# Optimization experiments

Hardware: AMD Instinct MI355X
Metric: run time of the kernel (lower is better)

## Reference

```python
import jax, jax.numpy as jnp
import numpy as np

B, M, N, F, H = 4, 512, 1024, 256, 256
K, K2, KC, RADIUS = 8, 4, 16, 0.5
EPS = 1e-5


def _cdist(a, b):
    d2 = (jnp.sum(a * a, -1)[..., :, None] + jnp.sum(b * b, -1)[..., None, :]
          - 2.0 * jnp.einsum('bnd,bmd->bnm', a, b))
    return jnp.sqrt(jnp.maximum(d2, 0.0))


def _scf_oe(xyz):
    # spherical coords (r, theta, phi) relative to cloud centroid -> (B,3,Npts)
    rel = xyz - jnp.mean(xyz, axis=1, keepdims=True)
    r = jnp.sqrt(jnp.sum(rel * rel, -1) + 1e-8)
    theta = jnp.arccos(jnp.clip(rel[..., 2] / r, -1.0, 1.0))
    phi = jnp.arctan2(rel[..., 1], rel[..., 0])
    return jnp.stack([r, theta, phi], axis=1)


def _knn_desc(xyz):
    # per-point SCF descriptor: sorted distances to KC nearest neighbors
    d = _cdist(xyz, xyz)
    return jnp.sort(d, axis=-1)[..., 1:KC + 1]


def _inorm(x):
    # InstanceNorm1d, affine=False: normalize over last dim per (b, row)
    mu = jnp.mean(x, -1, keepdims=True)
    var = jnp.var(x, -1, keepdims=True)
    return (x - mu) / jnp.sqrt(var + EPS)


def _conv1x1(x, W, g, b):
    # Conv2d 1x1 + BN(affine) + ReLU on (B,C,N,K)
    y = jnp.einsum('bcnk,oc->bonk', x, W)
    return jax.nn.relu(g[:, None, None] * y + b[:, None, None])


def _conv12(x, W, g, b):
    # Conv2d kernel (1,2) stride (1,2) + BN(affine) + ReLU on (B,C,N,P)
    Bb, C, Nn, P = x.shape
    xr = x.reshape(Bb, C, Nn, P // 2, 2)
    y = jnp.einsum('bcnpt,oct->bonp', xr, W)
    return jax.nn.relu(g[:, None, None] * y + b[:, None, None])


def _pointsift(xyz, feat, params):
    # PointSIFT OE: nearest neighbor in each of 8 octants within radius
    w1, g1, b1, w2, g2, b2, w3, g3, b3 = params
    Bb, Nn, _ = xyz.shape
    diff = xyz[:, None, :, :] - xyz[:, :, None, :]  # diff[b,i,j] = xyz[j]-xyz[i]
    d2 = jnp.sum(diff * diff, -1)
    octant = ((diff[..., 0] > 0).astype(jnp.int32) * 4
              + (diff[..., 1] > 0).astype(jnp.int32) * 2
              + (diff[..., 2] > 0).astype(jnp.int32))
    base = jnp.broadcast_to(jnp.arange(Nn)[None, :], (Bb, Nn))
    idxs = []
    for c in range(8):  # fixed small structural loop
        m = (octant == c) & (d2 <= RADIUS * RADIUS) & (d2 > 0)
        dm = jnp.where(m, d2, jnp.inf)
        j = jnp.argmin(dm, -1)
        valid = jnp.isfinite(jnp.min(dm, -1))
        idxs.append(jnp.where(valid, j, base))
    idx = jnp.stack(idxs, -1)  # (B,N,8)
    gxyz = jax.vmap(lambda p, i: p[i])(xyz, idx) - xyz[:, :, None, :]
    gfeat = jax.vmap(lambda f, i: f[i])(feat, idx)
    g = jnp.concatenate([gxyz, gfeat], -1).transpose(0, 3, 1, 2)  # (B,3+C,N,8)
    g = _conv12(g, w1, g1, b1)
    g = _conv12(g, w2, g2, b2)
    g = _conv12(g, w3, g3, b3)
    return g[..., 0]  # (B,C,N)


def setup_inputs():
    key = jax.random.key(0)
    ks = iter(jax.random.split(key, 64))
    rn = lambda shape, s=0.05: jax.random.normal(next(ks), shape, dtype=jnp.float32) * s
    ones = lambda shape: jnp.ones(shape, jnp.float32)
    zeros = lambda shape: jnp.zeros(shape, jnp.float32)
    inp = {
        'template_feature': rn((B, F, M), 1.0),
        'search_feature': rn((B, F, N), 1.0),
        'template_xyz': rn((B, M, 3), 1.0),
        'search_xyz': rn((B, N, 3), 1.0),
        'template_bc': rn((B, M, 9), 1.0),
        'search_bc': rn((B, N, 9), 1.0),
        'mlp_w1': rn((H, F + 3)), 'mlp_g1': ones(H), 'mlp_b1': zeros(H),
        'mlp_w2': rn((H, H)), 'mlp_g2': ones(H), 'mlp_b2': zeros(H),
        'mlp_w3': rn((H, H)), 'mlp_g3': ones(H), 'mlp_b3': zeros(H),
        'fea_w1': rn((F, H)), 'fea_g1': ones(F), 'fea_b1': zeros(F),
        'fea_w2': rn((F, F)), 'fea_bias2': zeros(F),
        'attn_wqkv': rn((3 * F, F)),
        'pos_w1': rn((64, 12)), 'pos_b1': zeros(64),
        'pos_w2': rn((F, 64)), 'pos_b2': zeros(F),
        'amlp_w1': rn((4 * F, F)), 'amlp_b1': zeros(4 * F),
        'amlp_w2': rn((F, 4 * F)), 'amlp_b2': zeros(F),
        'oe1_w1': rn((F, F + 3, 2)), 'oe1_g1': ones(F), 'oe1_b1': zeros(F),
        'oe1_w2': rn((F, F, 2)), 'oe1_g2': ones(F), 'oe1_b2': zeros(F),
        'oe1_w3': rn((F, F, 2)), 'oe1_g3': ones(F), 'oe1_b3': zeros(F),
        'oe2_w1': rn((F, F + 3, 2)), 'oe2_g1': ones(F), 'oe2_b1': zeros(F),
        'oe2_w2': rn((F, F, 2)), 'oe2_g2': ones(F), 'oe2_b2': zeros(F),
        'oe2_w3': rn((F, F, 2)), 'oe2_g3': ones(F), 'oe2_b3': zeros(F),
    }
    return inp


def reference(template_feature, search_feature, template_xyz, search_xyz, template_bc, search_bc,
              mlp_w1, mlp_g1, mlp_b1, mlp_w2, mlp_g2, mlp_b2, mlp_w3, mlp_g3, mlp_b3,
              fea_w1, fea_g1, fea_b1, fea_w2, fea_bias2,
              attn_wqkv, pos_w1, pos_b1, pos_w2, pos_b2, amlp_w1, amlp_b1, amlp_w2, amlp_b2,
              oe1_w1, oe1_g1, oe1_b1, oe1_w2, oe1_g2, oe1_b2, oe1_w3, oe1_g3, oe1_b3,
              oe2_w1, oe2_g1, oe2_b1, oe2_w2, oe2_g2, oe2_b2, oe2_w3, oe2_g3, oe2_b3):
    # ---- box-cloud distance + candidate pruning ----
    dist_bc = _cdist(template_bc, search_bc)  # (B,M,N)
    t_box = jnp.concatenate([template_xyz.transpose(0, 2, 1), template_bc.transpose(0, 2, 1),
                             template_feature, _scf_oe(template_xyz)], 1)  # (B,15+F,M)
    s_box = jnp.concatenate([search_xyz.transpose(0, 2, 1), search_bc.transpose(0, 2, 1),
                             search_feature, _scf_oe(search_xyz)], 1)      # (B,15+F,N)
    idx_b = jnp.argsort(dist_bc, axis=1)[:, :3 * K, :].transpose(0, 2, 1)  # (B,N,3K)
    dist_xyz = _cdist(search_xyz, template_xyz)  # (B,N,M)
    bi = jnp.arange(B)[:, None, None]
    ni = jnp.arange(N)[None, :, None]
    mask = jnp.full((B, N, M), 1e5, jnp.float32).at[bi, ni, idx_b].set(1.0)
    idx_k = jnp.argsort((dist_xyz * mask).transpose(0, 2, 1), axis=1)[:, :K, :].transpose(0, 2, 1)  # (B,N,K)
    # ---- SCF descriptor matching restricted to xyz candidates ----
    sd = _knn_desc(search_xyz)
    td = _knn_desc(template_xyz)
    mask2 = jnp.full((B, N, M), 1e5, jnp.float32).at[bi, ni, idx_k].set(1.0)
    dist_scf = _cdist(sd, td) * mask2
    idx_s = jnp.argsort(dist_scf.transpose(0, 2, 1), axis=1)[:, :K2, :].transpose(0, 2, 1)  # (B,N,K2)
    # ---- grouping + shared MLP ----
    corr = jax.vmap(lambda f, i: f[:, i])(t_box, idx_s)        # (B,15+F,N,K2)
    fused = jnp.concatenate([s_box[..., None], corr], -1)      # (B,15+F,N,K2+1)
    feats = fused.transpose(0, 2, 3, 1)[..., 12:]              # drop xyz+bc -> (B,N,K2+1,F+3)
    h = feats.transpose(0, 3, 1, 2)
    h = _conv1x1(h, mlp_w1, mlp_g1, mlp_b1)
    h = _conv1x1(h, mlp_w2, mlp_g2, mlp_b2)
    h = _conv1x1(h, mlp_w3, mlp_g3, mlp_b3)
    h = h.transpose(0, 2, 3, 1)                                # (B,N,K2+1,H)
    nn_xyz = corr[:, 0:3].transpose(0, 2, 3, 1)
    st_xyz = jnp.concatenate([search_xyz[:, :, None, :], nn_xyz], 2)
    nn_bc = corr[:, 3:12].transpose(0, 2, 3, 1)
    st_bc = jnp.concatenate([search_bc[:, :, None, :], nn_bc], 2)
    pos = jnp.concatenate([st_xyz, st_bc], -1)                 # (B,N,K2+1,12)
    KP1 = K2 + 1
    x = h.reshape(B * N, KP1, H)
    p = pos.reshape(B * N, KP1, 12)
    # ---- point transformer layer over tiny neighborhoods ----
    qkv = jnp.einsum('bnd,ed->bne', x, attn_wqkv)
    q, k, v = jnp.split(qkv, 3, axis=-1)
    rel_pos = p[:, :, None, :] - p[:, None, :, :]
    pe = jnp.einsum('bijp,hp->bijh', rel_pos, pos_w1) + pos_b1
    pe = jnp.einsum('bijh,dh->bijd', jax.nn.relu(pe), pos_w2) + pos_b2
    sim_in = q[:, :, None, :] - k[:, None, :, :] + pe
    hh = jax.nn.relu(jnp.einsum('bijd,hd->bijh', sim_in, amlp_w1) + amlp_b1)
    sim = jnp.einsum('bijh,dh->bijd', hh, amlp_w2) + amlp_b2
    attn = jax.nn.softmax(sim, axis=-2)
    agg = jnp.einsum('bijd,bijd->bid', attn, v[:, None, :, :] + pe)
    ff = agg.reshape(B, N, KP1, H).transpose(0, 3, 1, 2)[..., 0]  # (B,F,N)
    # ---- residual + instance norms + fea_layer ----
    ff = ff + search_feature
    ff = _inorm(ff.transpose(0, 2, 1)).transpose(0, 2, 1)
    y = jax.nn.relu(fea_g1[:, None] * jnp.einsum('bcn,oc->bon', ff, fea_w1) + fea_b1[:, None])
    y = jnp.einsum('bcn,oc->bon', y, fea_w2) + fea_bias2[:, None]
    y = _inorm((y + ff).transpose(0, 2, 1)).transpose(0, 2, 1)
    # ---- two PointSIFT OE modules with residuals ----
    y = y + _pointsift(search_xyz, y.transpose(0, 2, 1), (oe1_w1, oe1_g1, oe1_b1, oe1_w2, oe1_g2, oe1_b2, oe1_w3, oe1_g3, oe1_b3))
    y = y + _pointsift(search_xyz, y.transpose(0, 2, 1), (oe2_w1, oe2_g1, oe2_b1, oe2_w2, oe2_g2, oe2_b2, oe2_w3, oe2_g3, oe2_b3))
    return y
```

## Files before the change

kernel.cpp:

```cpp
#include <hip/hip_runtime.h>
#include <hip/hip_bf16.h>
#include <math.h>

constexpr int Bc = 4, Mc = 512, Nc = 1024, Fc = 256;
constexpr int KCc = 16;
constexpr float INFF = 3.0e38f;

typedef __attribute__((ext_vector_type(8))) short short8b;
typedef __attribute__((ext_vector_type(4))) float f32x4;

__device__ __forceinline__ short f2bf(float f) {
  __hip_bfloat16 h = __float2bfloat16(f);
  return *reinterpret_cast<short*>(&h);
}
__device__ __forceinline__ float bf2f(short s) {
  unsigned int u = ((unsigned int)(unsigned short)s) << 16;
  return __uint_as_float(u);
}
__device__ __forceinline__ unsigned long long umin64(unsigned long long a, unsigned long long b) {
  return a < b ? a : b;
}

__device__ __forceinline__ float blk_sum(float v, float* red) {
  int t = threadIdx.x;
// ... 34 lines not shown
    v = (k < 256) ? s.p[5][(size_t)(512 + r) * 256 + k] : pw2[(size_t)r * 64 + (k - 256)];
  else
    v = (k < K) ? s.p[job][(size_t)r * K + k] : 0.f;
  dstbase[gi] = f2bf(v);
}

__global__ __launch_bounds__(256) void scf_kernel(const float* __restrict__ xyz,
                                                  float* __restrict__ out, int P) {
  __shared__ float red[256];
  int b = blockIdx.x;
  const float* x = xyz + (size_t)b * P * 3;
  float sx = 0.f, sy = 0.f, sz = 0.f;
  for (int i = threadIdx.x; i < P; i += 256) {
    sx += x[3 * i]; sy += x[3 * i + 1]; sz += x[3 * i + 2];
  }
  float mx = blk_sum(sx, red) / (float)P;
  float my = blk_sum(sy, red) / (float)P;
  float mz = blk_sum(sz, red) / (float)P;
  for (int i = threadIdx.x; i < P; i += 256) {
    float a = x[3 * i] - mx, c = x[3 * i + 1] - my, d = x[3 * i + 2] - mz;
    float r = sqrtf(a * a + c * c + d * d + 1e-8f);
    float ct = d / r;
    ct = fminf(1.f, fmaxf(-1.f, ct));
    out[((size_t)b * 3 + 0) * P + i] = r;
    out[((size_t)b * 3 + 1) * P + i] = acosf(ct);
    out[((size_t)b * 3 + 2) * P + i] = atan2f(c, a);
  }
}

template <int P>
__global__ __launch_bounds__(256) void knn_kernel(const float* __restrict__ xyz,
                                                  float* __restrict__ desc) {
  constexpr int E = P / 64;
  int wv = threadIdx.x >> 6, l = threadIdx.x & 63;
  int pt = blockIdx.x * 4 + wv;
  int b = pt / P, i = pt % P;
  const float* x = xyz + (size_t)b * P * 3;
  float xi0 = x[3 * i], xi1 = x[3 * i + 1], xi2 = x[3 * i + 2];
  float d2r[E];
#pragma unroll
  for (int q = 0; q < E; ++q) {
    int j = q * 64 + l;
    float dx = x[3 * j] - xi0, dy = x[3 * j + 1] - xi1, dz = x[3 * j + 2] - xi2;
    d2r[q] = dx * dx + dy * dy + dz * dz;
  }
  for (int round = 0; round < KCc + 1; ++round) {
    unsigned long long k = ~0ULL;
#pragma unroll
    for (int q = 0; q < E; ++q) {
      unsigned long long c =
          ((unsigned long long)__float_as_uint(d2r[q]) << 32) | (unsigned)(q * 64 + l);
      k = umin64(k, c);
    }
#pragma unroll
    for (int m = 1; m < 64; m <<= 1) k = umin64(k, __shfl_xor(k, m));
    int widx = (int)(unsigned)k;
    if (round > 0 && l == 0)
      desc[((size_t)b * P + i) * KCc + (round - 1)] = sqrtf(__uint_as_float((unsigned)(k >> 32)));
    if ((widx & 63) == l) {
      int q = widx >> 6;
#pragma unroll
      for (int qq = 0; qq < E; ++qq)
        if (qq == q) d2r[qq] = INFF;
    }
  }
}

__global__ __launch_bounds__(256) void select_kernel(
    const float* __restrict__ tbc, const float* __restrict__ sbc,
    const float* __restrict__ txyz, const float* __restrict__ sxyz,
    const float* __restrict__ sd, const float* __restrict__ td,
    int* __restrict__ idx_s) {
  __shared__ int cand4[4][24];
  int wv = threadIdx.x >> 6, l = threadIdx.x & 63;
  int pt = blockIdx.x * 4 + wv;
  int b = pt / Nc, n = pt % Nc;
  const float* sb = sbc + ((size_t)b * Nc + n) * 9;
  float sreg[9];
#pragma unroll
  for (int c = 0; c < 9; ++c) sreg[c] = sb[c];
  float d2r[8];
#pragma unroll
  for (int q = 0; q < 8; ++q) {
    int m = q * 64 + l;
    const float* tb = tbc + ((size_t)b * Mc + m) * 9;
    float acc = 0.f;
#pragma unroll
    for (int c = 0; c < 9; ++c) { float d = tb[c] - sreg[c]; acc += d * d; }
    d2r[q] = acc;
  }
  for (int round = 0; round < 24; ++round) {
    unsigned long long k = ~0ULL;
#pragma unroll
    for (int q = 0; q < 8; ++q) {
      unsigned long long c =
          ((unsigned long long)__float_as_uint(d2r[q]) << 32) | (unsigned)(q * 64 + l);
      k = umin64(k, c);
    }
#pragma unroll
    for (int m = 1; m < 64; m <<= 1) k = umin64(k, __shfl_xor(k, m));
    int widx = (int)(unsigned)k;
    if (l == 0) cand4[wv][round] = widx;
    if ((widx & 63) == l) {
      int q = widx >> 6;
#pragma unroll
      for (int qq = 0; qq < 8; ++qq)
        if (qq == q) d2r[qq] = INFF;
    }
  }
  if (l == 0) {
    int* cand = cand4[wv];
    const float* sp = sxyz + ((size_t)b * Nc + n) * 3;
    float sx = sp[0], sy = sp[1], sz = sp[2];
    float dv[24];
    for (int t2 = 0; t2 < 24; ++t2) {
      const float* tp = txyz + ((size_t)b * Mc + cand[t2]) * 3;
      float dx = tp[0] - sx, dy = tp[1] - sy, dz = tp[2] - sz;
      dv[t2] = dx * dx + dy * dy + dz * dz;
    }
    int c8[8]; bool used[24];
    for (int t2 = 0; t2 < 24; ++t2) used[t2] = false;
    for (int r = 0; r < 8; ++r) {
      float bv = INFF; int bt = -1, bm = 0x7fffffff;
      for (int t2 = 0; t2 < 24; ++t2) {
        if (used[t2]) continue;
        int m = cand[t2];
        if (bt < 0 || dv[t2] < bv || (dv[t2] == bv && m < bm)) { bv = dv[t2]; bt = t2; bm = m; }
      }
      used[bt] = true; c8[r] = bm;
    }
    const float* sdp = sd + ((size_t)b * Nc + n) * KCc;
    float sdr[16];
    for (int t2 = 0; t2 < 16; ++t2) sdr[t2] = sdp[t2];
    float dscf[8];
    for (int r = 0; r < 8; ++r) {
      const float* tdp = td + ((size_t)b * Mc + c8[r]) * KCc;
      float acc = 0.f;
      for (int t2 = 0; t2 < 16; ++t2) { float d = sdr[t2] - tdp[t2]; acc += d * d; }
      dscf[r] = acc;
    }
    bool u8[8] = {false, false, false, false, false, false, false, false};
    for (int r = 0; r < 4; ++r) {
      float bv = INFF; int bt = -1, bm = 0x7fffffff;
      for (int t2 = 0; t2 < 8; ++t2) {
        if (u8[t2]) continue;
        if (bt < 0 || dscf[t2] < bv || (dscf[t2] == bv && c8[t2] < bm)) { bv = dscf[t2]; bt = t2; bm = c8[t2]; }
      }
      u8[bt] = true;
      idx_s[(((size_t)b * Nc + n) << 2) + r] = bm;
    }
  }
}

__global__ __launch_bounds__(256) void mlp_kernel(
    const float* __restrict__ sfeat, const float* __restrict__ tfeat,
    const float* __restrict__ sscf, const float* __restrict__ tscf,
    const int* __restrict__ idx_s,
    const short* __restrict__ w1f, const float* __restrict__ g1, const float* __restrict__ b1,
    const short* __restrict__ w2f, const float* __restrict__ g2, const float* __restrict__ b2,
    const short* __restrict__ w3f, const float* __restrict__ g3, const float* __restrict__ b3,
    short* __restrict__ houtS) {
  __shared__ __align__(16) char smem[34816];
  char* B1 = smem;
  char* B2 = smem + 18432;
  __shared__ int ms[16];
  int t = threadIdx.x;
  int tau0 = blockIdx.x * 4;
  int b = tau0 / Nc, n0 = tau0 % Nc;
  if (t < 16) ms[t] = idx_s[(((size_t)b * Nc + n0 + (t >> 2)) << 2) + (t & 3)];
  __syncthreads();
  for (int z = t; z < 32 * 29; z += 256) {
    int col = z / 29, k = 259 + z % 29;
    *(short*)(B1 + ((col * 576 + 2 * k) ^ ((col & 7) << 4))) = 0;
  }
  for (int z = t; z < 12 * 259; z += 256) {
    int col = 20 + z / 259, k = z % 259;
    *(short*)(B1 + ((col * 576 + 2 * k) ^ ((col & 7) << 4))) = 0;
  }
  for (int s = 0; s < 4; ++s) {
    int n = n0 + s;
    {
      int col = s * 5; int cx = (col & 7) << 4;
      *(short*)(B1 + ((col * 576 + t * 2) ^ cx)) = f2bf(sfeat[((size_t)b * Fc + t) * Nc + n]);
      if (t < 3) *(short*)(B1 + ((col * 576 + (256 + t) * 2) ^ cx)) = f2bf(sscf[((size_t)b * 3 + t) * Nc + n]);
    }
    for (int k = 1; k < 5; ++k) {
      int m = ms[s * 4 + k - 1];
      int col = s * 5 + k; int cx = (col & 7) << 4;
      *(short*)(B1 + ((col * 576 + t * 2) ^ cx)) = f2bf(tfeat[((size_t)b * Fc + t) * Mc + m]);
      if (t < 3) *(short*)(B1 + ((col * 576 + (256 + t) * 2) ^ cx)) = f2bf(tscf[((size_t)b * 3 + t) * Mc + m]);
    }
  }
  __syncthreads();
  int l = t & 63, w = t >> 6, lg = l >> 4, lr = l & 15;
  {
    f32x4 acc[4][2];
#pragma unroll
    for (int i = 0; i < 4; ++i) { acc[i][0] = (f32x4){0,0,0,0}; acc[i][1] = (f32x4){0,0,0,0}; }
    for (int kk = 0; kk < 9; ++kk) {
      int c1 = 16 + lr;
      short8b b0 = *(const short8b*)(B1 + ((lr * 576 + kk * 64 + lg * 16) ^ ((lr & 7) << 4)));
      short8b bb1 = *(const short8b*)(B1 + ((c1 * 576 + kk * 64 + lg * 16) ^ ((c1 & 7) << 4)));
#pragma unroll
      for (int i = 0; i < 4; ++i) {
        short8b a = *(const short8b*)(w1f + (((size_t)((w * 4 + i) * 9 + kk)) * 64 + l) * 8);
        acc[i][0] = __builtin_amdgcn_mfma_f32_16x16x32_bf16(a, b0, acc[i][0], 0, 0, 0);
        acc[i][1] = __builtin_amdgcn_mfma_f32_16x16x32_bf16(a, bb1, acc[i][1], 0, 0, 0);
      }
    }
    __syncthreads();
#pragma unroll
    for (int i = 0; i < 4; ++i) {
      int r0 = (w * 4 + i) * 16 + lg * 4;
      float4 gg = *(const float4*)(g1 + r0), bs = *(const float4*)(b1 + r0);
#pragma unroll
      for (int ct = 0; ct < 2; ++ct) {
        int col = ct * 16 + lr; int cx = (col & 7) << 4;
        ushort4 hv;
        hv.x = (unsigned short)f2bf(fmaxf(gg.x * acc[i][ct][0] + bs.x, 0.f));
        hv.y = (unsigned short)f2bf(fmaxf(gg.y * acc[i][ct][1] + bs.y, 0.f));
        hv.z = (unsigned short)f2bf(fmaxf(gg.z * acc[i][ct][2] + bs.z, 0.f));
        hv.w = (unsigned short)f2bf(fmaxf(gg.w * acc[i][ct][3] + bs.w, 0.f));
        *(ushort4*)(B2 + ((col * 512 + r0 * 2) ^ cx)) = hv;
      }
    }
  }
  __syncthreads();
  {
    f32x4 acc[4][2];
#pragma unroll
    for (int i = 0; i < 4; ++i) { acc[i][0] = (f32x4){0,0,0,0}; acc[i][1] = (f32x4){0,0,0,0}; }
    for (int kk = 0; kk < 8; ++kk) {
      int c1 = 16 + lr;
      short8b b0 = *(const short8b*)(B2 + ((lr * 512 + kk * 64 + lg * 16) ^ ((lr & 7) << 4)));
      short8b bb1 = *(const short8b*)(B2 + ((c1 * 512 + kk * 64 + lg * 16) ^ ((c1 & 7) << 4)));
#pragma unroll
      for (int i = 0; i < 4; ++i) {
        short8b a = *(const short8b*)(w2f + (((size_t)((w * 4 + i) * 8 + kk)) * 64 + l) * 8);
        acc[i][0] = __builtin_amdgcn_mfma_f32_16x16x32_bf16(a, b0, acc[i][0], 0, 0, 0);
        acc[i][1] = __builtin_amdgcn_mfma_f32_16x16x32_bf16(a, bb1, acc[i][1], 0, 0, 0);
      }
    }
    __syncthreads();
#pragma unroll
    for (int i = 0; i < 4; ++i) {
      int r0 = (w * 4 + i) * 16 + lg * 4;
      float4 gg = *(const float4*)(g2 + r0), bs = *(const float4*)(b2 + r0);
#pragma unroll
      for (int ct = 0; ct < 2; ++ct) {
        int col = ct * 16 + lr; int cx = (col & 7) << 4;
        ushort4 hv;
        hv.x = (unsigned short)f2bf(fmaxf(gg.x * acc[i][ct][0] + bs.x, 0.f));
        hv.y = (unsigned short)f2bf(fmaxf(gg.y * acc[i][ct][1] + bs.y, 0.f));
        hv.z = (unsigned short)f2bf(fmaxf(gg.z * acc[i][ct][2] + bs.z, 0.f));
        hv.w = (unsigned short)f2bf(fmaxf(gg.w * acc[i][ct][3] + bs.w, 0.f));
        *(ushort4*)(B1 + ((col * 512 + r0 * 2) ^ cx)) = hv;
      }
    }
  }
  __syncthreads();
  {
    f32x4 acc[4][2];
#pragma unroll
    for (int i = 0; i < 4; ++i) { acc[i][0] = (f32x4){0,0,0,0}; acc[i][1] = (f32x4){0,0,0,0}; }
    for (int kk = 0; kk < 8; ++kk) {
      int c1 = 16 + lr;
      short8b b0 = *(const short8b*)(B1 + ((lr * 512 + kk * 64 + lg * 16) ^ ((lr & 7) << 4)));
      short8b bb1 = *(const short8b*)(B1 + ((c1 * 512 + kk * 64 + lg * 16) ^ ((c1 & 7) << 4)));
#pragma unroll
      for (int i = 0; i < 4; ++i) {
        short8b a = *(const short8b*)(w3f + (((size_t)((w * 4 + i) * 8 + kk)) * 64 + l) * 8);
        acc[i][0] = __builtin_amdgcn_mfma_f32_16x16x32_bf16(a, b0, acc[i][0], 0, 0, 0);
        acc[i][1] = __builtin_amdgcn_mfma_f32_16x16x32_bf16(a, bb1, acc[i][1], 0, 0, 0);
      }
    }
#pragma unroll
    for (int i = 0; i < 4; ++i) {
      int r0 = (w * 4 + i) * 16 + lg * 4;
      float4 gg = *(const float4*)(g3 + r0), bs = *(const float4*)(b3 + r0);
#pragma unroll
      for (int ct = 0; ct < 2; ++ct) {
        int col = ct * 16 + lr;
        if (col < 20) {
          ushort4 hv;
          hv.x = (unsigned short)f2bf(fmaxf(gg.x * acc[i][ct][0] + bs.x, 0.f));
          hv.y = (unsigned short)f2bf(fmaxf(gg.y * acc[i][ct][1] + bs.y, 0.f));
          hv.z = (unsigned short)f2bf(fmaxf(gg.z * acc[i][ct][2] + bs.z, 0.f));
          hv.w = (unsigned short)f2bf(fmaxf(gg.w * acc[i][ct][3] + bs.w, 0.f));
          int s = col / 5, j = col % 5;
          *(ushort4*)(houtS + ((size_t)(tau0 + s) * 5 + j) * 256 + r0) = hv;
        }
      }
    }
  }
}

__global__ __launch_bounds__(512, 4) void attn_kernel(
    const short* __restrict__ hbufS, const int* __restrict__ idx_s,
    const float* __restrict__ sxyz, const float* __restrict__ sbc,
    const float* __restrict__ txyz, const float* __restrict__ tbc,
    const short* __restrict__ aqf, const short* __restrict__ akpef, const short* __restrict__ avpef,
    const float* __restrict__ pw1, const float* __restrict__ pb1, const float* __restrict__ pb2,
    const short* __restrict__ aw1f, const float* __restrict__ ab1,
    const short* __restrict__ aw2f, const float* __restrict__ ab2,
    const float* __restrict__ sfeat,
    const short* __restrict__ fw1f, const float* __restrict__ fg1, const float* __restrict__ fb1,
    const short* __restrict__ fw2f, const float* __restrict__ fb2v,
    float* __restrict__ yout) {
  __shared__ __align__(16) char smem[79872];
  char* Bx   = smem;
  char* vpeB = smem;
  char* feaB = smem;
  char* feaH = smem + 8192;
  float* y2F = (float*)(smem + 16384);
  char* KB   = smem + 30720;
  char* simS = smem + 30720;
  char* HpB  = smem + 55296;
  float* qF  = (float*)(smem + 55296);
  float* q04 = (float*)(smem + 55296);
  float* redf = (float*)(smem + 63488);
  float* pc4 = (float*)(smem + 64000);
  int t = threadIdx.x;
  int tau0 = blockIdx.x * 8;
  int b = tau0 / Nc, n0 = tau0 % Nc;
  int w = t >> 6, l = t & 63, lg = l >> 4, lr = l & 15;
  int h = t >> 8, ch = t & 255;
  for (int z = t; z < 2560; z += 512) {
    int col = 40 + z / 320, k = z % 320;
    *(short*)(Bx + ((col * 640 + 2 * k) ^ ((col & 7) << 4))) = 0;
  }
  for (int sj = h; sj < 40; sj += 2) {
    int s = sj / 5, j = sj % 5;
    *(short*)(Bx + ((sj * 640 + 2 * ch) ^ ((sj & 7) << 4))) =
        hbufS[(size_t)(tau0 + s) * 1280 + j * 256 + ch];
  }
  if (t < 40) {
    int s = t / 5, k = t % 5;
    int n = n0 + s;
    float* pd = pc4 + t * 12;
    if (k == 0) {
      for (int c = 0; c < 3; ++c) pd[c] = sxyz[((size_t)b * Nc + n) * 3 + c];
      for (int c = 0; c < 9; ++c) pd[3 + c] = sbc[((size_t)b * Nc + n) * 9 + c];
    } else {
      int m = idx_s[(((size_t)b * Nc + n) << 2) + (k - 1)];
      for (int c = 0; c < 3; ++c) pd[c] = txyz[((size_t)b * Mc + m) * 3 + c];
      for (int c = 0; c < 9; ++c) pd[3 + c] = tbc[((size_t)b * Mc + m) * 9 + c];
    }
  }
  __syncthreads();
  for (int it = t; it < 2560; it += 512) {
    int sj = it >> 6, hh = it & 63;
    int s = sj / 5;
    float acc = pb1[hh];
    const float* wv = pw1 + hh * 12;
    const float* p0 = pc4 + (s * 5) * 12;
    const float* pj = pc4 + sj * 12;
#pragma unroll
    for (int p = 0; p < 12; ++p) acc += wv[p] * (p0[p] - pj[p]);
    *(short*)(Bx + ((sj * 640 + 512 + 2 * hh) ^ ((sj & 7) << 4))) = f2bf(fmaxf(acc, 0.f));
  }
  __syncthreads();
  {
    f32x4 qA[2][3];
#pragma unroll
    for (int i = 0; i < 2; ++i)
#pragma unroll
      for (int ct = 0; ct < 3; ++ct) qA[i][ct] = (f32x4){0,0,0,0};
    for (int kk = 0; kk < 8; ++kk) {
      short8b bq[3];
#pragma unroll
      for (int ct = 0; ct < 3; ++ct) {
        int col = ct * 16 + lr;
        bq[ct] = *(const short8b*)(Bx + ((col * 640 + kk * 64 + lg * 16) ^ ((col & 7) << 4)));
      }
#pragma unroll
      for (int i = 0; i < 2; ++i) {
        short8b a = *(const short8b*)(aqf + (((size_t)((w * 2 + i) * 8 + kk)) * 64 + l) * 8);
#pragma unroll
        for (int ct = 0; ct < 3; ++ct)
          qA[i][ct] = __builtin_amdgcn_mfma_f32_16x16x32_bf16(a, bq[ct], qA[i][ct], 0, 0, 0);
      }
    }
#pragma unroll
    for (int i = 0; i < 2; ++i) {
      int r0 = (w * 2 + i) * 16 + lg * 4;
#pragma unroll
      for (int ct = 0; ct < 3; ++ct) {
        int col = ct * 16 + lr;
        if (col < 40 && col % 5 == 0)
          *(f32x4*)(qF + (col / 5) * 256 + r0) = qA[i][ct];
      }
    }
  }
  f32x4 sA[2][3], vA[2][3];
#pragma unroll
  for (int i = 0; i < 2; ++i)
#pragma unroll
    for (int ct = 0; ct < 3; ++ct) { sA[i][ct] = (f32x4){0,0,0,0}; vA[i][ct] = (f32x4){0,0,0,0}; }
  for (int kk = 0; kk < 10; ++kk) {
    short8b bb[3];
#pragma unroll
    for (int ct = 0; ct < 3; ++ct) {
      int col = ct * 16 + lr;
      bb[ct] = *(const short8b*)(Bx + ((col * 640 + kk * 64 + lg * 16) ^ ((col & 7) << 4)));
    }
#pragma unroll
    for (int i = 0; i < 2; ++i) {
      short8b ak = *(const short8b*)(akpef + (((size_t)((w * 2 + i) * 10 + kk)) * 64 + l) * 8);
      short8b av = *(const short8b*)(avpef + (((size_t)((w * 2 + i) * 10 + kk)) * 64 + l) * 8);
#pragma unroll
      for (int ct = 0; ct < 3; ++ct) {
        sA[i][ct] = __builtin_amdgcn_mfma_f32_16x16x32_bf16(ak, bb[ct], sA[i][ct], 0, 0, 0);
        vA[i][ct] = __builtin_amdgcn_mfma_f32_16x16x32_bf16(av, bb[ct], vA[i][ct], 0, 0, 0);
      }
    }
  }
  __syncthreads();
#pragma unroll
  for (int i = 0; i < 2; ++i) {
    int r0 = (w * 2 + i) * 16 + lg * 4;
    float4 pb = *(const float4*)(pb2 + r0);
#pragma unroll
    for (int ct = 0; ct < 3; ++ct) {
      int col = ct * 16 + lr; int cx = (col & 7) << 4;
      if (col < 40) {
        int s = col / 5;
        f32x4 qv = *(const f32x4*)(qF + s * 256 + r0);
        ushort4 kv, vv;
        kv.x = (unsigned short)f2bf(qv[0] + sA[i][ct][0] + pb.x);
        kv.y = (unsigned short)f2bf(qv[1] + sA[i][ct][1] + pb.y);
        kv.z = (unsigned short)f2bf(qv[2] + sA[i][ct][2] + pb.z);
        kv.w = (unsigned short)f2bf(qv[3] + sA[i][ct][3] + pb.w);
        vv.x = (unsigned short)f2bf(vA[i][ct][0] + pb.x);
        vv.y = (unsigned short)f2bf(vA[i][ct][1] + pb.y);
        vv.z = (unsigned short)f2bf(vA[i][ct][2] + pb.z);
        vv.w = (unsigned short)f2bf(vA[i][ct][3] + pb.w);
// ... 262 lines not shown
    sidx[(((size_t)b * Nc + i) << 3) + l] = j;
  }
}

__global__ __launch_bounds__(512, 4) void sift_oe_kernel(
    const float* __restrict__ sxyz, const int* __restrict__ sidx,
    const float* __restrict__ yin,
    const short* __restrict__ w1f, const float* __restrict__ g1, const float* __restrict__ b1,
    const short* __restrict__ w2f, const float* __restrict__ g2, const float* __restrict__ b2,
    const short* __restrict__ w3f, const float* __restrict__ g3, const float* __restrict__ b3,
    float* __restrict__ yout) {
  __shared__ __align__(16) char smem[51200];
  char* B1 = smem;
  char* B2 = smem + 34816;
  char* B3 = smem;
  __shared__ int js[8][8];
  int t = threadIdx.x;
  int i0 = blockIdx.x * 8;
  int b = i0 / Nc, nb = i0 % Nc;
  int h = t >> 8, ch = t & 255;
  if (t < 64) js[t >> 3][t & 7] = sidx[(((size_t)b * Nc + nb + (t >> 3)) << 3) + (t & 7)];
  for (int z = t; z < 32 * 26; z += 512) {
    int col = z / 26, k = 518 + z % 26;
    *(short*)(B1 + ((col * 1088 + 2 * k) ^ ((col & 7) << 4))) = 0;
  }
  __syncthreads();
  for (int si = 0; si < 4; ++si) {
    int s = h * 4 + si;
    int ii = nb + s;
#pragma unroll
    for (int p = 0; p < 4; ++p) {
      int ja = js[s][2 * p], jb = js[s][2 * p + 1];
      int col = s * 4 + p; int cx = (col & 7) << 4;
      float va = yin[((size_t)b * Nc + ja) * 256 + ch];
      float vb = yin[((size_t)b * Nc + jb) * 256 + ch];
      unsigned int packed = (unsigned int)(unsigned short)f2bf(va) |
                            ((unsigned int)(unsigned short)f2bf(vb) << 16);
      *(unsigned int*)(B1 + ((col * 1088 + 12 + 4 * ch) ^ cx)) = packed;
      if (ch < 3) {
        float base = sxyz[((size_t)b * Nc + ii) * 3 + ch];
        float ga = sxyz[((size_t)b * Nc + ja) * 3 + ch] - base;
        float gb = sxyz[((size_t)b * Nc + jb) * 3 + ch] - base;
        unsigned int pg = (unsigned int)(unsigned short)f2bf(ga) |
                          ((unsigned int)(unsigned short)f2bf(gb) << 16);
        *(unsigned int*)(B1 + ((col * 1088 + 4 * ch) ^ cx)) = pg;
      }
    }
  }
  __syncthreads();
  int l = t & 63, w = t >> 6, lg = l >> 4, lr = l & 15;
  {
    f32x4 acc[2][2];
#pragma unroll
    for (int i = 0; i < 2; ++i) { acc[i][0] = (f32x4){0,0,0,0}; acc[i][1] = (f32x4){0,0,0,0}; }
    for (int kk = 0; kk < 17; ++kk) {
      short8b b0[2];
#pragma unroll
      for (int ct = 0; ct < 2; ++ct) {
        int col = ct * 16 + lr;
        b0[ct] = *(const short8b*)(B1 + ((col * 1088 + kk * 64 + lg * 16) ^ ((col & 7) << 4)));
      }
#pragma unroll
      for (int i = 0; i < 2; ++i) {
        short8b a = *(const short8b*)(w1f + (((size_t)((w * 2 + i) * 17 + kk)) * 64 + l) * 8);
#pragma unroll
        for (int ct = 0; ct < 2; ++ct)
          acc[i][ct] = __builtin_amdgcn_mfma_f32_16x16x32_bf16(a, b0[ct], acc[i][ct], 0, 0, 0);
      }
    }
    __syncthreads();
#pragma unroll
    for (int i = 0; i < 2; ++i) {
      int r0 = (w * 2 + i) * 16 + lg * 4;
      float4 gg = *(const float4*)(g1 + r0), bs = *(const float4*)(b1 + r0);
#pragma unroll
      for (int ct = 0; ct < 2; ++ct) {
        int col = ct * 16 + lr;
        int s = col >> 2, p = col & 3, p2 = p >> 1, tp = p & 1;
        int col2 = s * 2 + p2; int cx2 = (col2 & 7) << 4;
        *(short*)(B2 + ((col2 * 1024 + (2 * r0 + tp) * 2) ^ cx2)) =
            f2bf(fmaxf(gg.x * acc[i][ct][0] + bs.x, 0.f));
        *(short*)(B2 + ((col2 * 1024 + (2 * (r0 + 1) + tp) * 2) ^ cx2)) =
            f2bf(fmaxf(gg.y * acc[i][ct][1] + bs.y, 0.f));
        *(short*)(B2 + ((col2 * 1024 + (2 * (r0 + 2) + tp) * 2) ^ cx2)) =
            f2bf(fmaxf(gg.z * acc[i][ct][2] + bs.z, 0.f));
        *(short*)(B2 + ((col2 * 1024 + (2 * (r0 + 3) + tp) * 2) ^ cx2)) =
            f2bf(fmaxf(gg.w * acc[i][ct][3] + bs.w, 0.f));
      }
    }
  }
  __syncthreads();
  {
    f32x4 acc[2];
#pragma unroll
    for (int i = 0; i < 2; ++i) acc[i] = (f32x4){0,0,0,0};
    for (int kk = 0; kk < 16; ++kk) {
      short8b b0 = *(const short8b*)(B2 + ((lr * 1024 + kk * 64 + lg * 16) ^ ((lr & 7) << 4)));
#pragma unroll
      for (int i = 0; i < 2; ++i) {
        short8b a = *(const short8b*)(w2f + (((size_t)((w * 2 + i) * 16 + kk)) * 64 + l) * 8);
        acc[i] = __builtin_amdgcn_mfma_f32_16x16x32_bf16(a, b0, acc[i], 0, 0, 0);
      }
    }
    __syncthreads();
    int s = lr >> 1, tp = lr & 1;
    int col3 = s; int cx3 = (col3 & 7) << 4;
#pragma unroll
    for (int i = 0; i < 2; ++i) {
      int r0 = (w * 2 + i) * 16 + lg * 4;
      float4 gg = *(const float4*)(g2 + r0), bs = *(const float4*)(b2 + r0);
      *(short*)(B3 + ((col3 * 1024 + (2 * r0 + tp) * 2) ^ cx3)) =
          f2bf(fmaxf(gg.x * acc[i][0] + bs.x, 0.f));
      *(short*)(B3 + ((col3 * 1024 + (2 * (r0 + 1) + tp) * 2) ^ cx3)) =
          f2bf(fmaxf(gg.y * acc[i][1] + bs.y, 0.f));
      *(short*)(B3 + ((col3 * 1024 + (2 * (r0 + 2) + tp) * 2) ^ cx3)) =
          f2bf(fmaxf(gg.z * acc[i][2] + bs.z, 0.f));
      *(short*)(B3 + ((col3 * 1024 + (2 * (r0 + 3) + tp) * 2) ^ cx3)) =
          f2bf(fmaxf(gg.w * acc[i][3] + bs.w, 0.f));
    }
  }
  __syncthreads();
  {
    f32x4 acc[2];
#pragma unroll
    for (int i = 0; i < 2; ++i) acc[i] = (f32x4){0,0,0,0};
    for (int kk = 0; kk < 16; ++kk) {
      short8b b0 = *(const short8b*)(B3 + ((lr * 1024 + kk * 64 + lg * 16) ^ ((lr & 7) << 4)));
#pragma unroll
      for (int i = 0; i < 2; ++i) {
        short8b a = *(const short8b*)(w3f + (((size_t)((w * 2 + i) * 16 + kk)) * 64 + l) * 8);
        acc[i] = __builtin_amdgcn_mfma_f32_16x16x32_bf16(a, b0, acc[i], 0, 0, 0);
      }
    }
#pragma unroll
    for (int i = 0; i < 2; ++i) {
      if (lr < 8) {
        int s = lr;
        int r0 = (w * 2 + i) * 16 + lg * 4;
        float4 gg = *(const float4*)(g3 + r0), bs = *(const float4*)(b3 + r0);
        float4 yv = *(const float4*)(yin + ((size_t)(i0 + s)) * 256 + r0);
        float4 ov;
        ov.x = yv.x + fmaxf(gg.x * acc[i][0] + bs.x, 0.f);
        ov.y = yv.y + fmaxf(gg.y * acc[i][1] + bs.y, 0.f);
        ov.z = yv.z + fmaxf(gg.z * acc[i][2] + bs.z, 0.f);
        ov.w = yv.w + fmaxf(gg.w * acc[i][3] + bs.w, 0.f);
        *(float4*)(yout + ((size_t)(i0 + s)) * 256 + r0) = ov;
      }
    }
  }
}

__global__ __launch_bounds__(256) void transpose_kernel(const float* __restrict__ yin,
                                                        float* __restrict__ out) {
  size_t idx = (size_t)blockIdx.x * 256 + threadIdx.x;
  int n = (int)(idx % Nc);
  size_t r = idx / Nc;
  int c = (int)(r % Fc);
  int b = (int)(r / Fc);
  out[idx] = yin[(((size_t)b * Nc + n) * 256) + c];
}

extern "C" void kernel_launch(void* const* d_in, const int* in_sizes, int n_in,
                              void* d_out, int out_size, void* d_ws, size_t ws_size,
                              hipStream_t stream) {
  (void)in_sizes; (void)n_in; (void)out_size; (void)ws_size;
  const float* tfeat = (const float*)d_in[0];
  const float* sfeat = (const float*)d_in[1];
  const float* txyz  = (const float*)d_in[2];
  const float* sxyz  = (const float*)d_in[3];
  const float* tbc   = (const float*)d_in[4];
  const float* sbc   = (const float*)d_in[5];
  const float* mw1 = (const float*)d_in[6];
  const float* mg1 = (const float*)d_in[7];
  const float* mb1 = (const float*)d_in[8];
  const float* mw2 = (const float*)d_in[9];
  const float* mg2 = (const float*)d_in[10];
  const float* mb2 = (const float*)d_in[11];
  const float* mw3 = (const float*)d_in[12];
  const float* mg3 = (const float*)d_in[13];
  const float* mb3 = (const float*)d_in[14];
  const float* fw1 = (const float*)d_in[15];
  const float* fg1 = (const float*)d_in[16];
  const float* fb1 = (const float*)d_in[17];
  const float* fw2 = (const float*)d_in[18];
  const float* fb2 = (const float*)d_in[19];
  const float* wqkv = (const float*)d_in[20];
  const float* pw1 = (const float*)d_in[21];
  const float* pb1 = (const float*)d_in[22];
  const float* pw2 = (const float*)d_in[23];
  const float* pb2 = (const float*)d_in[24];
  const float* aw1 = (const float*)d_in[25];
  const float* ab1 = (const float*)d_in[26];
  const float* aw2 = (const float*)d_in[27];
  const float* ab2 = (const float*)d_in[28];
  const float* o1w1 = (const float*)d_in[29];
  const float* o1g1 = (const float*)d_in[30];
  const float* o1b1 = (const float*)d_in[31];
  const float* o1w2 = (const float*)d_in[32];
  const float* o1g2 = (const float*)d_in[33];
  const float* o1b2 = (const float*)d_in[34];
  const float* o1w3 = (const float*)d_in[35];
  const float* o1g3 = (const float*)d_in[36];
  const float* o1b3 = (const float*)d_in[37];
  const float* o2w1 = (const float*)d_in[38];
  const float* o2g1 = (const float*)d_in[39];
  const float* o2b1 = (const float*)d_in[40];
  const float* o2w2 = (const float*)d_in[41];
  const float* o2g2 = (const float*)d_in[42];
  const float* o2b2 = (const float*)d_in[43];
  const float* o2w3 = (const float*)d_in[44];
  const float* o2g3 = (const float*)d_in[45];
  const float* o2b3 = (const float*)d_in[46];

  float* ws = (float*)d_ws;
  float* sd   = ws;
  float* td   = sd + 65536;
  float* sscf = td + 32768;
  float* tscf = sscf + 12288;
  int*   idxs = (int*)(tscf + 6144);
  int*   sidx = idxs + 16384;
  float* yws  = (float*)(sidx + 32768);
  short* sb   = (short*)(yws + 1048576);
  short* hbufS = sb;
  short* mw1f  = sb + 5242880;
  short* mw2f  = mw1f + 73728;
  short* mw3f  = mw2f + 65536;
  short* aqf   = mw3f + 65536;
  short* akpef = aqf + 65536;
  short* avpef = akpef + 81920;
  short* aw1f  = avpef + 81920;
  short* aw2f  = aw1f + 262144;
  short* fw1f  = aw2f + 262144;
  short* fw2f  = fw1f + 65536;
  short* o1w1f = fw2f + 65536;
  short* o1w2f = o1w1f + 139264;
  short* o1w3f = o1w2f + 131072;
  short* o2w1f = o1w3f + 131072;
  short* o2w2f = o2w1f + 139264;
  short* o2w3f = o2w2f + 131072;
  float* ybuf2 = (float*)sb;

  WSrcs srcs;
  srcs.p[0] = mw1;  srcs.p[1] = mw2;  srcs.p[2] = mw3;  srcs.p[3] = wqkv;
  srcs.p[4] = wqkv; srcs.p[5] = wqkv; srcs.p[6] = aw1;  srcs.p[7] = aw2;
  srcs.p[8] = fw1;  srcs.p[9] = fw2;  srcs.p[10] = o1w1; srcs.p[11] = o1w2;
  srcs.p[12] = o1w3; srcs.p[13] = o2w1; srcs.p[14] = o2w2; srcs.p[15] = o2w3;
  wconv_all<<<7392, 256, 0, stream>>>(srcs, pw2, mw1f);

  scf_kernel<<<Bc, 256, 0, stream>>>(sxyz, sscf, Nc);
  scf_kernel<<<Bc, 256, 0, stream>>>(txyz, tscf, Mc);
  knn_kernel<Nc><<<Bc * Nc / 4, 256, 0, stream>>>(sxyz, sd);
  knn_kernel<Mc><<<Bc * Mc / 4, 256, 0, stream>>>(txyz, td);
  select_kernel<<<Bc * Nc / 4, 256, 0, stream>>>(tbc, sbc, txyz, sxyz, sd, td, idxs);
  mlp_kernel<<<Bc * Nc / 4, 256, 0, stream>>>(sfeat, tfeat, sscf, tscf, idxs,
                                              mw1f, mg1, mb1, mw2f, mg2, mb2,
                                              mw3f, mg3, mb3, hbufS);
  attn_kernel<<<Bc * Nc / 8, 512, 0, stream>>>(hbufS, idxs, sxyz, sbc, txyz, tbc,
                                               aqf, akpef, avpef, pw1, pb1, pb2,
                                               aw1f, ab1, aw2f, ab2,
                                               sfeat, fw1f, fg1, fb1, fw2f, fb2, yws);
  sift_idx_kernel<<<Bc * Nc / 4, 256, 0, stream>>>(sxyz, sidx);
  sift_oe_kernel<<<Bc * Nc / 8, 512, 0, stream>>>(sxyz, sidx, yws,
                                                  o1w1f, o1g1, o1b1, o1w2f, o1g2, o1b2,
                                                  o1w3f, o1g3, o1b3, ybuf2);
  sift_oe_kernel<<<Bc * Nc / 8, 512, 0, stream>>>(sxyz, sidx, ybuf2,
                                                  o2w1f, o2g1, o2b1, o2w2f, o2g2, o2b2,
                                                  o2w3f, o2g3, o2b3, yws);
  transpose_kernel<<<(Bc * Fc * Nc) / 256, 256, 0, stream>>>(yws, (float*)d_out);
}
```

Measured before the change: 339.3 us.

## Process eight points per MLP block with 512 threads; tile the output transpose

The MLP kernel now handles 8 query points (40 columns padded to 48) per 512-thread block. Each wave computes 2 row tiles by 3 column tiles, so every weight fragment loaded from global memory feeds three MFMAs instead of two and the padding waste drops from 12/32 to 8/48 columns. The final transpose now goes through a 64x64 LDS tile, so both the reads and the writes are coalesced instead of strided. The cost is more LDS per block (about 51 KB), which may limit how many blocks fit on a CU.

```diff
diff --git a/kernel.cpp b/kernel.cpp
--- a/kernel.cpp
+++ b/kernel.cpp
@@ -210,7 +210,7 @@
   }
 }
 
-__global__ __launch_bounds__(256) void mlp_kernel(
+__global__ __launch_bounds__(512, 4) void mlp_kernel(
     const float* __restrict__ sfeat, const float* __restrict__ tfeat,
     const float* __restrict__ sscf, const float* __restrict__ tscf,
     const int* __restrict__ idx_s,
@@ -218,61 +218,70 @@
     const short* __restrict__ w2f, const float* __restrict__ g2, const float* __restrict__ b2,
     const short* __restrict__ w3f, const float* __restrict__ g3, const float* __restrict__ b3,
     short* __restrict__ houtS) {
-  __shared__ __align__(16) char smem[34816];
+  __shared__ __align__(16) char smem[52224];
   char* B1 = smem;
-  char* B2 = smem + 18432;
-  __shared__ int ms[16];
+  char* B2 = smem + 27648;
+  char* B3 = smem;
+  __shared__ int ms[32];
   int t = threadIdx.x;
-  int tau0 = blockIdx.x * 4;
+  int tau0 = blockIdx.x * 8;
   int b = tau0 / Nc, n0 = tau0 % Nc;
-  if (t < 16) ms[t] = idx_s[(((size_t)b * Nc + n0 + (t >> 2)) << 2) + (t & 3)];
-  __syncthreads();
-  for (int z = t; z < 32 * 29; z += 256) {
+  int h = t >> 8, ch = t & 255;
+  if (t < 32) ms[t] = idx_s[(((size_t)b * Nc + n0 + (t >> 2)) << 2) + (t & 3)];
+  __syncthreads();
+  for (int z = t; z < 48 * 29; z += 512) {
     int col = z / 29, k = 259 + z % 29;
     *(short*)(B1 + ((col * 576 + 2 * k) ^ ((col & 7) << 4))) = 0;
   }
-  for (int z = t; z < 12 * 259; z += 256) {
-    int col = 20 + z / 259, k = z % 259;
+  for (int z = t; z < 8 * 259; z += 512) {
+    int col = 40 + z / 259, k = z % 259;
     *(short*)(B1 + ((col * 576 + 2 * k) ^ ((col & 7) << 4))) = 0;
   }
-  for (int s = 0; s < 4; ++s) {
+  for (int sj = h; sj < 40; sj += 2) {
+    int s = sj / 5, j = sj % 5;
     int n = n0 + s;
-    {
-      int col = s * 5; int cx = (col & 7) << 4;
-      *(short*)(B1 + ((col * 576 + t * 2) ^ cx)) = f2bf(sfeat[((size_t)b * Fc + t) * Nc + n]);
-      if (t < 3) *(short*)(B1 + ((col * 576 + (256 + t) * 2) ^ cx)) = f2bf(sscf[((size_t)b * 3 + t) * Nc + n]);
-    }
-    for (int k = 1; k < 5; ++k) {
-      int m = ms[s * 4 + k - 1];
-      int col = s * 5 + k; int cx = (col & 7) << 4;
-      *(short*)(B1 + ((col * 576 + t * 2) ^ cx)) = f2bf(tfeat[((size_t)b * Fc + t) * Mc + m]);
-      if (t < 3) *(short*)(B1 + ((col * 576 + (256 + t) * 2) ^ cx)) = f2bf(tscf[((size_t)b * 3 + t) * Mc + m]);
+    int cx = (sj & 7) << 4;
+    if (j == 0) {
+      *(short*)(B1 + ((sj * 576 + 2 * ch) ^ cx)) = f2bf(sfeat[((size_t)b * Fc + ch) * Nc + n]);
+      if (ch < 3)
+        *(short*)(B1 + ((sj * 576 + (256 + ch) * 2) ^ cx)) = f2bf(sscf[((size_t)b * 3 + ch) * Nc + n]);
+    } else {
+      int m = ms[s * 4 + j - 1];
+      *(short*)(B1 + ((sj * 576 + 2 * ch) ^ cx)) = f2bf(tfeat[((size_t)b * Fc + ch) * Mc + m]);
+      if (ch < 3)
+        *(short*)(B1 + ((sj * 576 + (256 + ch) * 2) ^ cx)) = f2bf(tscf[((size_t)b * 3 + ch) * Mc + m]);
     }
   }
   __syncthreads();
   int l = t & 63, w = t >> 6, lg = l >> 4, lr = l & 15;
   {
-    f32x4 acc[4][2];
-#pragma unroll
-    for (int i = 0; i < 4; ++i) { acc[i][0] = (f32x4){0,0,0,0}; acc[i][1] = (f32x4){0,0,0,0}; }
+    f32x4 acc[2][3];
+#pragma unroll
+    for (int i = 0; i < 2; ++i)
+#pragma unroll
+      for (int ct = 0; ct < 3; ++ct) acc[i][ct] = (f32x4){0,0,0,0};
     for (int kk = 0; kk < 9; ++kk) {
-      int c1 = 16 + lr;
-      short8b b0 = *(const short8b*)(B1 + ((lr * 576 + kk * 64 + lg * 16) ^ ((lr & 7) << 4)));
-      short8b bb1 = *(const short8b*)(B1 + ((c1 * 576 + kk * 64 + lg * 16) ^ ((c1 & 7) << 4)));
-#pragma unroll
-      for (int i = 0; i < 4; ++i) {
-        short8b a = *(const short8b*)(w1f + (((size_t)((w * 4 + i) * 9 + kk)) * 64 + l) * 8);
-        acc[i][0] = __builtin_amdgcn_mfma_f32_16x16x32_bf16(a, b0, acc[i][0], 0, 0, 0);
-        acc[i][1] = __builtin_amdgcn_mfma_f32_16x16x32_bf16(a, bb1, acc[i][1], 0, 0, 0);
+      short8b bb[3];
+#pragma unroll
+      for (int ct = 0; ct < 3; ++ct) {
+        int col = ct * 16 + lr;
+        bb[ct] = *(const short8b*)(B1 + ((col * 576 + kk * 64 + lg * 16) ^ ((col & 7) << 4)));
+      }
+#pragma unroll
+      for (int i = 0; i < 2; ++i) {
+        short8b a = *(const short8b*)(w1f + (((size_t)((w * 2 + i) * 9 + kk)) * 64 + l) * 8);
+#pragma unroll
+        for (int ct = 0; ct < 3; ++ct)
+          acc[i][ct] = __builtin_amdgcn_mfma_f32_16x16x32_bf16(a, bb[ct], acc[i][ct], 0, 0, 0);
       }
     }
     __syncthreads();
 #pragma unroll
-    for (int i = 0; i < 4; ++i) {
-      int r0 = (w * 4 + i) * 16 + lg * 4;
+    for (int i = 0; i < 2; ++i) {
+      int r0 = (w * 2 + i) * 16 + lg * 4;
       float4 gg = *(const float4*)(g1 + r0), bs = *(const float4*)(b1 + r0);
 #pragma unroll
-      for (int ct = 0; ct < 2; ++ct) {
+      for (int ct = 0; ct < 3; ++ct) {
         int col = ct * 16 + lr; int cx = (col & 7) << 4;
         ushort4 hv;
         hv.x = (unsigned short)f2bf(fmaxf(gg.x * acc[i][ct][0] + bs.x, 0.f));
@@ -285,61 +294,73 @@
   }
   __syncthreads();
   {
-    f32x4 acc[4][2];
-#pragma unroll
-    for (int i = 0; i < 4; ++i) { acc[i][0] = (f32x4){0,0,0,0}; acc[i][1] = (f32x4){0,0,0,0}; }
+    f32x4 acc[2][3];
+#pragma unroll
+    for (int i = 0; i < 2; ++i)
+#pragma unroll
+      for (int ct = 0; ct < 3; ++ct) acc[i][ct] = (f32x4){0,0,0,0};
     for (int kk = 0; kk < 8; ++kk) {
-      int c1 = 16 + lr;
-      short8b b0 = *(const short8b*)(B2 + ((lr * 512 + kk * 64 + lg * 16) ^ ((lr & 7) << 4)));
-      short8b bb1 = *(const short8b*)(B2 + ((c1 * 512 + kk * 64 + lg * 16) ^ ((c1 & 7) << 4)));
-#pragma unroll
-      for (int i = 0; i < 4; ++i) {
-        short8b a = *(const short8b*)(w2f + (((size_t)((w * 4 + i) * 8 + kk)) * 64 + l) * 8);
-        acc[i][0] = __builtin_amdgcn_mfma_f32_16x16x32_bf16(a, b0, acc[i][0], 0, 0, 0);
-        acc[i][1] = __builtin_amdgcn_mfma_f32_16x16x32_bf16(a, bb1, acc[i][1], 0, 0, 0);
+      short8b bb[3];
+#pragma unroll
+      for (int ct = 0; ct < 3; ++ct) {
+        int col = ct * 16 + lr;
+        bb[ct] = *(const short8b*)(B2 + ((col * 512 + kk * 64 + lg * 16) ^ ((col & 7) << 4)));
+      }
+#pragma unroll
+      for (int i = 0; i < 2; ++i) {
+        short8b a = *(const short8b*)(w2f + (((size_t)((w * 2 + i) * 8 + kk)) * 64 + l) * 8);
+#pragma unroll
+        for (int ct = 0; ct < 3; ++ct)
+          acc[i][ct] = __builtin_amdgcn_mfma_f32_16x16x32_bf16(a, bb[ct], acc[i][ct], 0, 0, 0);
       }
     }
     __syncthreads();
 #pragma unroll
-    for (int i = 0; i < 4; ++i) {
-      int r0 = (w * 4 + i) * 16 + lg * 4;
+    for (int i = 0; i < 2; ++i) {
+      int r0 = (w * 2 + i) * 16 + lg * 4;
       float4 gg = *(const float4*)(g2 + r0), bs = *(const float4*)(b2 + r0);
 #pragma unroll
-      for (int ct = 0; ct < 2; ++ct) {
+      for (int ct = 0; ct < 3; ++ct) {
         int col = ct * 16 + lr; int cx = (col & 7) << 4;
         ushort4 hv;
         hv.x = (unsigned short)f2bf(fmaxf(gg.x * acc[i][ct][0] + bs.x, 0.f));
         hv.y = (unsigned short)f2bf(fmaxf(gg.y * acc[i][ct][1] + bs.y, 0.f));
         hv.z = (unsigned short)f2bf(fmaxf(gg.z * acc[i][ct][2] + bs.z, 0.f));
         hv.w = (unsigned short)f2bf(fmaxf(gg.w * acc[i][ct][3] + bs.w, 0.f));
-        *(ushort4*)(B1 + ((col * 512 + r0 * 2) ^ cx)) = hv;
+        *(ushort4*)(B3 + ((col * 512 + r0 * 2) ^ cx)) = hv;
       }
     }
   }
   __syncthreads();
   {
-    f32x4 acc[4][2];
-#pragma unroll
-    for (int i = 0; i < 4; ++i) { acc[i][0] = (f32x4){0,0,0,0}; acc[i][1] = (f32x4){0,0,0,0}; }
+    f32x4 acc[2][3];
+#pragma unroll
+    for (int i = 0; i < 2; ++i)
+#pragma unroll
+      for (int ct = 0; ct < 3; ++ct) acc[i][ct] = (f32x4){0,0,0,0};
     for (int kk = 0; kk < 8; ++kk) {
-      int c1 = 16 + lr;
-      short8b b0 = *(const short8b*)(B1 + ((lr * 512 + kk * 64 + lg * 16) ^ ((lr & 7) << 4)));
-      short8b bb1 = *(const short8b*)(B1 + ((c1 * 512 + kk * 64 + lg * 16) ^ ((c1 & 7) << 4)));
-#pragma unroll
-      for (int i = 0; i < 4; ++i) {
-        short8b a = *(const short8b*)(w3f + (((size_t)((w * 4 + i) * 8 + kk)) * 64 + l) * 8);
-        acc[i][0] = __builtin_amdgcn_mfma_f32_16x16x32_bf16(a, b0, acc[i][0], 0, 0, 0);
-        acc[i][1] = __builtin_amdgcn_mfma_f32_16x16x32_bf16(a, bb1, acc[i][1], 0, 0, 0);
-      }
-    }
-#pragma unroll
-    for (int i = 0; i < 4; ++i) {
-      int r0 = (w * 4 + i) * 16 + lg * 4;
+      short8b bb[3];
+#pragma unroll
+      for (int ct = 0; ct < 3; ++ct) {
+        int col = ct * 16 + lr;
+        bb[ct] = *(const short8b*)(B3 + ((col * 512 + kk * 64 + lg * 16) ^ ((col & 7) << 4)));
+      }
+#pragma unroll
+      for (int i = 0; i < 2; ++i) {
+        short8b a = *(const short8b*)(w3f + (((size_t)((w * 2 + i) * 8 + kk)) * 64 + l) * 8);
+#pragma unroll
+        for (int ct = 0; ct < 3; ++ct)
+          acc[i][ct] = __builtin_amdgcn_mfma_f32_16x16x32_bf16(a, bb[ct], acc[i][ct], 0, 0, 0);
+      }
+    }
+#pragma unroll
+    for (int i = 0; i < 2; ++i) {
+      int r0 = (w * 2 + i) * 16 + lg * 4;
       float4 gg = *(const float4*)(g3 + r0), bs = *(const float4*)(b3 + r0);
 #pragma unroll
-      for (int ct = 0; ct < 2; ++ct) {
+      for (int ct = 0; ct < 3; ++ct) {
         int col = ct * 16 + lr;
-        if (col < 20) {
+        if (col < 40) {
           ushort4 hv;
           hv.x = (unsigned short)f2bf(fmaxf(gg.x * acc[i][ct][0] + bs.x, 0.f));
           hv.y = (unsigned short)f2bf(fmaxf(gg.y * acc[i][ct][1] + bs.y, 0.f));
@@ -908,12 +929,24 @@
 
 __global__ __launch_bounds__(256) void transpose_kernel(const float* __restrict__ yin,
                                                         float* __restrict__ out) {
-  size_t idx = (size_t)blockIdx.x * 256 + threadIdx.x;
-  int n = (int)(idx % Nc);
-  size_t r = idx / Nc;
-  int c = (int)(r % Fc);
-  int b = (int)(r / Fc);
-  out[idx] = yin[(((size_t)b * Nc + n) * 256) + c];
+  __shared__ float tile[64][65];
+  int bid = blockIdx.x;
+  int b = bid >> 6;
+  int tl = bid & 63;
+  int n0 = (tl >> 2) * 64;
+  int c0 = (tl & 3) * 64;
+  int tx = threadIdx.x & 63, ty = threadIdx.x >> 6;
+#pragma unroll
+  for (int r = 0; r < 16; ++r) {
+    int i = r * 4 + ty;
+    tile[i][tx] = yin[((size_t)b * Nc + n0 + i) * 256 + c0 + tx];
+  }
+  __syncthreads();
+#pragma unroll
+  for (int r = 0; r < 16; ++r) {
+    int j = r * 4 + ty;
+    out[((size_t)b * Fc + c0 + j) * Nc + n0 + tx] = tile[tx][j];
+  }
 }
 
 extern "C" void kernel_launch(void* const* d_in, const int* in_sizes, int n_in,
@@ -1008,7 +1041,7 @@
   knn_kernel<Nc><<<Bc * Nc / 4, 256, 0, stream>>>(sxyz, sd);
   knn_kernel<Mc><<<Bc * Mc / 4, 256, 0, stream>>>(txyz, td);
   select_kernel<<<Bc * Nc / 4, 256, 0, stream>>>(tbc, sbc, txyz, sxyz, sd, td, idxs);
-  mlp_kernel<<<Bc * Nc / 4, 256, 0, stream>>>(sfeat, tfeat, sscf, tscf, idxs,
+  mlp_kernel<<<Bc * Nc / 8, 512, 0, stream>>>(sfeat, tfeat, sscf, tscf, idxs,
                                               mw1f, mg1, mb1, mw2f, mg2, mb2,
                                               mw3f, mg3, mb3, hbufS);
   attn_kernel<<<Bc * Nc / 8, 512, 0, stream>>>(hbufS, idxs, sxyz, sbc, txyz, tbc,
@@ -1022,5 +1055,5 @@
   sift_oe_kernel<<<Bc * Nc / 8, 512, 0, stream>>>(sxyz, sidx, ybuf2,
                                                   o2w1f, o2g1, o2b1, o2w2f, o2g2, o2b2,
                                                   o2w3f, o2g3, o2b3, yws);
-  transpose_kernel<<<(Bc * Fc * Nc) / 256, 256, 0, stream>>>(yws, (float*)d_out);
-}
+  transpose_kernel<<<256, 256, 0, stream>>>(yws, (float*)d_out);
+}
```

Result: faster. 315.9 us (-6.9%).
